# Optimization experiments

Hardware: AMD Instinct MI355X
Metric: run time of the kernel (lower is better)

The kernel has to match this reference:

```python
import jax, jax.numpy as jnp
import numpy as np

L = 2        # n_layers
D = 128      # embed_dim
H = 4        # n_heads
HD = D // H  # head_dim
B = 2
N = 4096
PERIOD = 2.0
WINDOW = 0.5
EPS = 1e-5
NF = D // 4  # n_frequencies = embed_dim / (n_dimensions * 2), n_dimensions=2


def setup_inputs() -> dict:
    key = jax.random.key(0)
    ks = jax.random.split(key, 12)
    s = 0.05  # weight init scale
    inp = {
        'x': jax.random.normal(ks[0], (B, N, D), jnp.float32),
        'pos': jax.random.uniform(ks[1], (B, N, 2), jnp.float32),
        'Wq_w': jax.random.normal(ks[2], (L, D, D), jnp.float32) * s,
        'Wq_b': jnp.zeros((L, D), jnp.float32),
        'Wk_w': jax.random.normal(ks[3], (L, D, D), jnp.float32) * s,
        'Wk_b': jnp.zeros((L, D), jnp.float32),
        'Wv_w': jax.random.normal(ks[4], (L, D, D), jnp.float32) * s,
        'Wv_b': jnp.zeros((L, D), jnp.float32),
        'Wo_w': jax.random.normal(ks[5], (L, D, D), jnp.float32) * s,
        'Wo_b': jnp.zeros((L, D), jnp.float32),
        'n1_g': jnp.ones((L, D), jnp.float32),
        'n1_b': jnp.zeros((L, D), jnp.float32),
        'n2_g': jnp.ones((L, D), jnp.float32),
        'n2_b': jnp.zeros((L, D), jnp.float32),
        'l1_w': jax.random.normal(ks[6], (L, D, 2 * D), jnp.float32) * s,
        'l1_b': jnp.zeros((L, 2 * D), jnp.float32),
        'l2_w': jax.random.normal(ks[7], (L, 2 * D, D), jnp.float32) * s,
        'l2_b': jnp.zeros((L, D), jnp.float32),
    }
    return inp


def _batchnorm(x, g, b):
    # BatchNorm1d in training mode over flattened (B*N, D)
    Bb, Nn, Dd = x.shape
    x2 = x.reshape(Bb * Nn, Dd)
    mu = x2.mean(0)
    var = x2.var(0)
    y = (x2 - mu) * jax.lax.rsqrt(var + EPS) * g + b
    return y.reshape(Bb, Nn, Dd)


def _rope(x, pos, freqs):
    # x: (B,N,D), pos: (B,N,2), freqs: (NF,)
    angle = pos[..., None] * freqs            # (B,N,2,NF)
    angle = jnp.repeat(angle, 2, axis=-1)     # (B,N,2,2*NF)
    angle = angle.reshape(x.shape)            # (B,N,D)
    xp = x.reshape(*x.shape[:-1], D // 2, 2)
    x_sw = jnp.stack([-xp[..., 1], xp[..., 0]], axis=-1).reshape(x.shape)
    return jnp.cos(angle) * x + jnp.sin(angle) * x_sw


def _forward(x, pos, Wq_w, Wq_b, Wk_w, Wk_b, Wv_w, Wv_b, Wo_w, Wo_b,
             n1_g, n1_b, n2_g, n2_b, l1_w, l1_b, l2_w, l2_b):
    freqs = 2 * jnp.pi * jnp.arange(1, NF + 1, dtype=x.dtype) / PERIOD
    # window mask: dist(i,j) <= WINDOW/2  -> compare squared distances
    sq = jnp.sum(pos * pos, axis=-1)                          # (B,N)
    d2 = sq[:, :, None] + sq[:, None, :] - 2 * jnp.einsum('bnd,bmd->bnm', pos, pos)
    mask = (d2 <= (WINDOW / 2) ** 2)[:, None, :, :]           # (B,1,N,N)
    scale = 1.0 / jnp.sqrt(jnp.asarray(HD, x.dtype))

    for i in range(L):
        xn = _batchnorm(x, n1_g[i], n1_b[i])
        q = xn @ Wq_w[i] + Wq_b[i]
        k = xn @ Wk_w[i] + Wk_b[i]
        v = xn @ Wv_w[i] + Wv_b[i]
        if i == 0:  # rotary encoding applied at first layer only
            q = _rope(q, pos, freqs)
            k = _rope(k, pos, freqs)
        # split heads: (B,N,D) -> (B,H,N,HD)
        qh = q.reshape(B, N, H, HD).transpose(0, 2, 1, 3)
        kh = k.reshape(B, N, H, HD).transpose(0, 2, 1, 3)
        vh = v.reshape(B, N, H, HD).transpose(0, 2, 1, 3)
        scores = jnp.einsum('bhnd,bhmd->bhnm', qh, kh) * scale
        scores = jnp.where(mask, scores, jnp.finfo(x.dtype).min)
        attn = jax.nn.softmax(scores, axis=-1)
        oh = jnp.einsum('bhnm,bhmd->bhnd', attn, vh)
        o = oh.transpose(0, 2, 1, 3).reshape(B, N, D)
        x = x + (o @ Wo_w[i] + Wo_b[i])
        # FFN block
        xn2 = _batchnorm(x, n2_g[i], n2_b[i])
        h = jax.nn.relu(xn2 @ l1_w[i] + l1_b[i])
        x = x + (h @ l2_w[i] + l2_b[i])
    return x


def reference(x, pos, Wq_w, Wq_b, Wk_w, Wk_b, Wv_w, Wv_b, Wo_w, Wo_b,
              n1_g, n1_b, n2_g, n2_b, l1_w, l1_b, l2_w, l2_b):
    return _forward(x, pos, Wq_w, Wq_b, Wk_w, Wk_b, Wv_w, Wv_b, Wo_w, Wo_b,
                    n1_g, n1_b, n2_g, n2_b, l1_w, l1_b, l2_w, l2_b)
```

## Files before the change

### kernel.cpp

```cpp
#include <hip/hip_runtime.h>
#include <hip/hip_bf16.h>
#include <math.h>

#define LYR 2
#define DIM 128
#define NH 4
#define HD 32
#define BB 2
#define NN 4096
#define MROWS (BB * NN)
#define R2 0.0625f
#define BN_EPS 1e-5f
#define CLOG2E 0.25503594f
#define NCH 4
#define CHLEN (NN / NCH)

typedef __attribute__((ext_vector_type(4))) float f32x4;
typedef __attribute__((ext_vector_type(8))) short bf16x8;
typedef __attribute__((ext_vector_type(4))) short bf16x4;

static __device__ inline unsigned short f2bf(float f) {
  union { float f; unsigned u; } v; v.f = f;
  unsigned r = v.u + 0x7FFFu + ((v.u >> 16) & 1u);
  return (unsigned short)(r >> 16);
}

static __device__ inline float exp2_fast(float x) {
#if defined(__has_builtin)
#if __has_builtin(__builtin_amdgcn_exp2f)
  return __builtin_amdgcn_exp2f(x);
#else
  return exp2f(x);
#endif
#else
  return exp2f(x);
#endif
}

static __device__ inline unsigned cvt_pk_bf16(float lo, float hi) {
  unsigned r;
  asm volatile("v_cvt_pk_bf16_f32 %0, %1, %2" : "=v"(r) : "v"(lo), "v"(hi));
  return r;
}

__global__ __launch_bounds__(256) void wprep_k(const float* __restrict__ Wq,
                                               const float* __restrict__ Wk,
                                               const float* __restrict__ Wv,
                                               const float* __restrict__ Wo,
                                               const float* __restrict__ L1,
                                               const float* __restrict__ L2,
                                               const float* __restrict__ Wqb,
                                               const float* __restrict__ Wkb,
                                               const float* __restrict__ Wvb,
                                               short* __restrict__ wT,
                                               float* __restrict__ qkvb) {
  const int id = blockIdx.x;
  const int l = id >> 7, r = id & 127;
  const size_t lbase = (size_t)l * 131072;
  const float* src; short* dst; int K, N, tk, tn;
  float mult = 1.0f;
  if (r < 64) {
    const int m = r >> 4, tile = r & 15;
    if (m == 0)      { src = Wq + (size_t)l * 16384; mult = CLOG2E; }
    else if (m == 1) src = Wk + (size_t)l * 16384;
    else if (m == 2) src = Wv + (size_t)l * 16384;
    else             src = Wo + (size_t)l * 16384;
    dst = wT + lbase + (size_t)m * 16384;
    K = 128; N = 128; tk = tile >> 2; tn = tile & 3;
  } else if (r < 96) {
    const int tile = r - 64;
    src = L1 + (size_t)l * 32768; dst = wT + lbase + 65536;
    K = 128; N = 256; tk = tile >> 3; tn = tile & 7;
  } else {
    const int tile = r - 96;
    src = L2 + (size_t)l * 32768; dst = wT + lbase + 98304;
    K = 256; N = 128; tk = tile >> 2; tn = tile & 3;
  }
  __shared__ float tl[32][33];
  const int t = threadIdx.x;
  const int rr = t >> 3, c4 = (t & 7) * 4;
  float4 vv = *(const float4*)(src + (size_t)(tk * 32 + rr) * N + tn * 32 + c4);
  tl[rr][c4 + 0] = vv.x; tl[rr][c4 + 1] = vv.y;
  tl[rr][c4 + 2] = vv.z; tl[rr][c4 + 3] = vv.w;
  __syncthreads();
  bf16x4 o4;
  o4[0] = (short)f2bf(tl[c4 + 0][rr] * mult);
  o4[1] = (short)f2bf(tl[c4 + 1][rr] * mult);
  o4[2] = (short)f2bf(tl[c4 + 2][rr] * mult);
  o4[3] = (short)f2bf(tl[c4 + 3][rr] * mult);
  *(bf16x4*)(dst + (size_t)(tn * 32 + rr) * K + tk * 32 + c4) = o4;
  if (r == 0) {
    for (int i = t; i < 384; i += 256) {
      float bv;
      if (i < 128)      bv = Wqb[l * 128 + i] * CLOG2E;
      else if (i < 256) bv = Wkb[l * 128 + i - 128];
      else              bv = Wvb[l * 128 + i - 256];
      qkvb[l * 384 + i] = bv;
    }
  }
}

__global__ __launch_bounds__(256) void copy_stats_k(const float* __restrict__ x,
                                                    float* __restrict__ out,
                                                    float* __restrict__ sums) {
  __shared__ float ss[8][128], sq[8][128];
  const int t = threadIdx.x;
  const int c4 = (t & 31) * 4, rg = t >> 5;
  const size_t base = (size_t)blockIdx.x * (32 * DIM);
  float s0 = 0.f, s1 = 0.f, s2 = 0.f, s3 = 0.f;
  float q0 = 0.f, q1 = 0.f, q2 = 0.f, q3 = 0.f;
  for (int r = rg; r < 32; r += 8) {
    float4 v = *(const float4*)&x[base + (size_t)r * DIM + c4];
    *(float4*)&out[base + (size_t)r * DIM + c4] = v;
    s0 += v.x; q0 += v.x * v.x;
    s1 += v.y; q1 += v.y * v.y;
    s2 += v.z; q2 += v.z * v.z;
    s3 += v.w; q3 += v.w * v.w;
  }
  ss[rg][c4 + 0] = s0; sq[rg][c4 + 0] = q0;
  ss[rg][c4 + 1] = s1; sq[rg][c4 + 1] = q1;
  ss[rg][c4 + 2] = s2; sq[rg][c4 + 2] = q2;
  ss[rg][c4 + 3] = s3; sq[rg][c4 + 3] = q3;
  __syncthreads();
  if (t < 128) {
    float S = 0.f, Q = 0.f;
#pragma unroll
    for (int r2 = 0; r2 < 8; r2++) { S += ss[r2][t]; Q += sq[r2][t]; }
    atomicAdd(&sums[t], S);
    atomicAdd(&sums[128 + t], Q);
  }
}

template <int MODE, bool RELU, bool ABN>
__global__ __launch_bounds__(256) void gemm_bf_k(const short* __restrict__ A,
                                                 const float* __restrict__ Af,
                                                 const float* __restrict__ stats,
                                                 const float* __restrict__ gma,
                                                 const float* __restrict__ btaN,
                                                 const short* __restrict__ WT,
                                                 const float* __restrict__ bias,
                                                 const float* res,
                                                 float* Cf,
                                                 short* __restrict__ Cb,
                                                 float* __restrict__ statsums,
                                                 int K) {
  __shared__ short a_s[64 * 80];
  __shared__ short w_s[64 * 80];
  __shared__ float sc_s[128], sh_s[128];
  const int t = threadIdx.x, w = t >> 6, lane = t & 63, g = lane >> 4, i16 = lane & 15;
  const int bm = blockIdx.x * 64, bn = blockIdx.y * 64;
  const int sr = t >> 2, sc = (t & 3) * 8, c16 = (t & 3) * 16;
  const size_t MN = (size_t)MROWS * DIM;
  if (ABN) {
    if (t < 128) {
      const float inv = 1.0f / (float)MROWS;
      const float mu = stats[t] * inv;
      const float var = stats[128 + t] * inv - mu * mu;
      const float rs = rsqrtf(var + BN_EPS);
      const float s = rs * gma[t];
      sc_s[t] = s;
      sh_s[t] = btaN[t] - mu * s;
    }
  }
  f32x4 acc[4];
#pragma unroll
  for (int ct = 0; ct < 4; ct++) acc[ct] = (f32x4){0.f, 0.f, 0.f, 0.f};
  for (int k0 = 0; k0 < K; k0 += 64) {
    __syncthreads();
    if (ABN) {
      const float* ap = Af + (size_t)(bm + sr) * K + k0 + c16;
      float4 x0 = *(const float4*)ap, x1 = *(const float4*)(ap + 4);
      float4 x2 = *(const float4*)(ap + 8), x3 = *(const float4*)(ap + 12);
      const int kb = k0 + c16;
      bf16x8 o0, o1;
      o0[0] = (short)f2bf(x0.x * sc_s[kb + 0]  + sh_s[kb + 0]);
      o0[1] = (short)f2bf(x0.y * sc_s[kb + 1]  + sh_s[kb + 1]);
      o0[2] = (short)f2bf(x0.z * sc_s[kb + 2]  + sh_s[kb + 2]);
      o0[3] = (short)f2bf(x0.w * sc_s[kb + 3]  + sh_s[kb + 3]);
      o0[4] = (short)f2bf(x1.x * sc_s[kb + 4]  + sh_s[kb + 4]);
      o0[5] = (short)f2bf(x1.y * sc_s[kb + 5]  + sh_s[kb + 5]);
      o0[6] = (short)f2bf(x1.z * sc_s[kb + 6]  + sh_s[kb + 6]);
      o0[7] = (short)f2bf(x1.w * sc_s[kb + 7]  + sh_s[kb + 7]);
      o1[0] = (short)f2bf(x2.x * sc_s[kb + 8]  + sh_s[kb + 8]);
      o1[1] = (short)f2bf(x2.y * sc_s[kb + 9]  + sh_s[kb + 9]);
      o1[2] = (short)f2bf(x2.z * sc_s[kb + 10] + sh_s[kb + 10]);
      o1[3] = (short)f2bf(x2.w * sc_s[kb + 11] + sh_s[kb + 11]);
      o1[4] = (short)f2bf(x3.x * sc_s[kb + 12] + sh_s[kb + 12]);
      o1[5] = (short)f2bf(x3.y * sc_s[kb + 13] + sh_s[kb + 13]);
      o1[6] = (short)f2bf(x3.z * sc_s[kb + 14] + sh_s[kb + 14]);
      o1[7] = (short)f2bf(x3.w * sc_s[kb + 15] + sh_s[kb + 15]);
      *(bf16x8*)&a_s[sr * 80 + c16] = o0;
      *(bf16x8*)&a_s[sr * 80 + c16 + 8] = o1;
    } else {
      *(bf16x8*)&a_s[sr * 80 + sc]      = *(const bf16x8*)(A + (size_t)(bm + sr) * K + k0 + sc);
      *(bf16x8*)&a_s[sr * 80 + sc + 32] = *(const bf16x8*)(A + (size_t)(bm + sr) * K + k0 + sc + 32);
    }
    *(bf16x8*)&w_s[sr * 80 + sc]      = *(const bf16x8*)(WT + (size_t)(bn + sr) * K + k0 + sc);
    *(bf16x8*)&w_s[sr * 80 + sc + 32] = *(const bf16x8*)(WT + (size_t)(bn + sr) * K + k0 + sc + 32);
    __syncthreads();
#pragma unroll
    for (int ks = 0; ks < 2; ks++) {
      bf16x8 af = *(const bf16x8*)&a_s[(16 * w + i16) * 80 + ks * 32 + 8 * g];
#pragma unroll
      for (int ct = 0; ct < 4; ct++) {
        bf16x8 wf = *(const bf16x8*)&w_s[(ct * 16 + i16) * 80 + ks * 32 + 8 * g];
        acc[ct] = __builtin_amdgcn_mfma_f32_16x16x32_bf16(af, wf, acc[ct], 0, 0, 0);
      }
    }
  }
  float s_acc[4], q_acc[4];
#pragma unroll
  for (int ct = 0; ct < 4; ct++) {
    const int col = bn + ct * 16 + i16;
    const float bv = bias[col];
    if (MODE == 3) {
      const int row0 = bm + 16 * w + 4 * g;
      if (col < 256) {
        short* dstb = (col < 128) ? Cb : (Cb + MN);
        const int cc = col & 127;
#pragma unroll
        for (int r = 0; r < 4; r++)
          dstb[(size_t)(row0 + r) * DIM + cc] = (short)f2bf(acc[ct][r] + bv);
      } else {
        const int b_ = row0 >> 12, n_ = row0 & (NN - 1);
        const int hh = (col - 256) >> 5, dd = (col - 256) & 31;
        bf16x4 o4;
#pragma unroll
        for (int r = 0; r < 4; r++) o4[r] = (short)f2bf(acc[ct][r] + bv);
        *(bf16x4*)(Cb + 2 * MN + ((size_t)(b_ * NH + hh) * HD + dd) * NN + n_) = o4;
      }
    } else if (MODE == 0) {
      float ssum = 0.f, qsum = 0.f;
#pragma unroll
      for (int r = 0; r < 4; r++) {
        const int row = bm + 16 * w + 4 * g + r;
        float vv = acc[ct][r] + bv + res[(size_t)row * DIM + col];
        Cf[(size_t)row * DIM + col] = vv;
        ssum += vv; qsum += vv * vv;
      }
      s_acc[ct] = ssum; q_acc[ct] = qsum;
    } else {
#pragma unroll
      for (int r = 0; r < 4; r++) {
        const int row = bm + 16 * w + 4 * g + r;
        float vv = acc[ct][r] + bv;
        if (RELU) vv = fmaxf(vv, 0.f);
        Cb[(size_t)row * (size_t)256 + col] = (short)f2bf(vv);
      }
    }
  }
  if (MODE == 0) {
#pragma unroll
    for (int ct = 0; ct < 4; ct++) {
      s_acc[ct] += __shfl_xor(s_acc[ct], 16, 64);
      s_acc[ct] += __shfl_xor(s_acc[ct], 32, 64);
      q_acc[ct] += __shfl_xor(q_acc[ct], 16, 64);
      q_acc[ct] += __shfl_xor(q_acc[ct], 32, 64);
    }
    float* bs = (float*)a_s;
    __syncthreads();
    if (t < 128) bs[t] = 0.f;
    __syncthreads();
    if (lane < 16) {
#pragma unroll
      for (int ct = 0; ct < 4; ct++) {
        atomicAdd(&bs[ct * 16 + i16], s_acc[ct]);
        atomicAdd(&bs[64 + ct * 16 + i16], q_acc[ct]);
      }
    }
    __syncthreads();
    if (t < 64) {
      atomicAdd(&statsums[bn + t], bs[t]);
      atomicAdd(&statsums[128 + bn + t], bs[64 + t]);
    }
  }
}

__global__ __launch_bounds__(256) void rope_bf_k(short* __restrict__ q,
                                                 short* __restrict__ kk,
                                                 const float* __restrict__ pos) {
  const int idx = blockIdx.x * 256 + threadIdx.x;
  const int row = idx >> 2, hh = idx & 3;
  const float2 pp = *(const float2*)&pos[(size_t)row * 2];
  short* qp = q + (size_t)row * DIM + hh * HD;
  short* kp = kk + (size_t)row * DIM + hh * HD;
  bf16x8 qv[4], kv[4];
#pragma unroll
  for (int u = 0; u < 4; u++) {
    qv[u] = *(const bf16x8*)(qp + 8 * u);
    kv[u] = *(const bf16x8*)(kp + 8 * u);
  }
#pragma unroll
  for (int lp = 0; lp < 16; lp++) {
    const int p = hh * 16 + lp;
    const float coord = (p < 32) ? pp.x : pp.y;
    const int f = p & 31;
    float sn, cs;
    __sincosf(3.14159265358979323846f * (float)(f + 1) * coord, &sn, &cs);
    const int u = lp >> 2, e = (lp & 3) * 2;
    const float a0 = __uint_as_float(((unsigned)(unsigned short)qv[u][e]) << 16);
    const float a1 = __uint_as_float(((unsigned)(unsigned short)qv[u][e + 1]) << 16);
    qv[u][e]     = (short)f2bf(cs * a0 - sn * a1);
    qv[u][e + 1] = (short)f2bf(cs * a1 + sn * a0);
    const float b0 = __uint_as_float(((unsigned)(unsigned short)kv[u][e]) << 16);
    const float b1 = __uint_as_float(((unsigned)(unsigned short)kv[u][e + 1]) << 16);
    kv[u][e]     = (short)f2bf(cs * b0 - sn * b1);
    kv[u][e + 1] = (short)f2bf(cs * b1 + sn * b0);
  }
#pragma unroll
  for (int u = 0; u < 4; u++) {
    *(bf16x8*)(qp + 8 * u) = qv[u];
    *(bf16x8*)(kp + 8 * u) = kv[u];
  }
}

__global__ __launch_bounds__(128) void attn4_k(const short* __restrict__ q,
                                               const short* __restrict__ k,
                                               const short* __restrict__ vt,
                                               const float* __restrict__ pos,
                                               float* __restrict__ accP,
                                               float* __restrict__ lP) {
  const int bh = blockIdx.y, b = bh >> 2, h = bh & 3;
  const int q0 = blockIdx.x * 32;
  const int ch = blockIdx.z;
  const int kbeg = ch * CHLEN, kend = kbeg + CHLEN;
  __shared__ short ks_s[64 * 40];
  __shared__ short vt_s[32 * 72];
  __shared__ short ps_s[2 * 16 * 72];
  __shared__ float pkx[64], pky[64], pnt[64];
  const int t = threadIdx.x, w = t >> 6, lane = t & 63, g = lane >> 4, i16 = lane & 15;
  const short* kp = k + (size_t)b * NN * DIM + h * HD;
  const short* vp = vt + (size_t)bh * HD * NN;

  const bf16x8 qf = *(const bf16x8*)(q + (size_t)(b * NN + q0 + 16 * w + i16) * DIM + h * HD + 8 * g);
  const float2 qp2 = *(const float2*)&pos[((size_t)b * NN + q0 + 16 * w + i16) * 2];
  const float qx = qp2.x, qy = qp2.y;
  const float ci = 0.5f * (qx * qx + qy * qy) - 0.5f * R2;

  bf16x8 kreg0 = *(const bf16x8*)(kp + (size_t)(kbeg + (t >> 2)) * DIM + (t & 3) * 8);
  bf16x8 kreg1 = *(const bf16x8*)(kp + (size_t)(kbeg + 32 + (t >> 2)) * DIM + (t & 3) * 8);
  bf16x8 vreg0 = *(const bf16x8*)(vp + (size_t)(t >> 3) * NN + kbeg + (t & 7) * 8);
  bf16x8 vreg1 = *(const bf16x8*)(vp + (size_t)((t >> 3) + 16) * NN + kbeg + (t & 7) * 8);
  float2 kpos = make_float2(0.f, 0.f);
  if (t < 64) kpos = *(const float2*)&pos[((size_t)b * NN + kbeg + t) * 2];

  f32x4 acc0 = {0.f, 0.f, 0.f, 0.f}, acc1 = {0.f, 0.f, 0.f, 0.f};
  const f32x4 zf = {0.f, 0.f, 0.f, 0.f};
  float l_run = 0.f;

  for (int k0 = kbeg; k0 < kend; k0 += 64) {
    __syncthreads();
    *(bf16x8*)&ks_s[(t >> 2) * 40 + (t & 3) * 8] = kreg0;
    *(bf16x8*)&ks_s[((t >> 2) + 32) * 40 + (t & 3) * 8] = kreg1;
    *(bf16x8*)&vt_s[(t >> 3) * 72 + (t & 7) * 8] = vreg0;
    *(bf16x8*)&vt_s[((t >> 3) + 16) * 72 + (t & 7) * 8] = vreg1;
    if (t < 64) {
      pkx[t] = kpos.x; pky[t] = kpos.y;
      pnt[t] = -0.5f * (kpos.x * kpos.x + kpos.y * kpos.y);
    }
    __syncthreads();
    const int kn = k0 + 64;
    if (kn < kend) {
      kreg0 = *(const bf16x8*)(kp + (size_t)(kn + (t >> 2)) * DIM + (t & 3) * 8);
      kreg1 = *(const bf16x8*)(kp + (size_t)(kn + 32 + (t >> 2)) * DIM + (t & 3) * 8);
      vreg0 = *(const bf16x8*)(vp + (size_t)(t >> 3) * NN + kn + (t & 7) * 8);
      vreg1 = *(const bf16x8*)(vp + (size_t)((t >> 3) + 16) * NN + kn + (t & 7) * 8);
      if (t < 64) kpos = *(const float2*)&pos[((size_t)b * NN + kn + t) * 2];
    }

    f32x4 sx[4];
#pragma unroll
    for (int jt = 0; jt < 4; jt++) {
      bf16x8 kf = *(const bf16x8*)&ks_s[(16 * jt + i16) * 40 + 8 * g];
      sx[jt] = __builtin_amdgcn_mfma_f32_16x16x32_bf16(kf, qf, zf, 0, 0, 0);
    }

    float pr[16];
    float tsum = 0.f;
#pragma unroll
    for (int jt = 0; jt < 4; jt++) {
      float4 kx4 = *(const float4*)&pkx[16 * jt + 4 * g];
      float4 ky4 = *(const float4*)&pky[16 * jt + 4 * g];
      float4 nt4 = *(const float4*)&pnt[16 * jt + 4 * g];
      const float kxa[4] = {kx4.x, kx4.y, kx4.z, kx4.w};
      const float kya[4] = {ky4.x, ky4.y, ky4.z, ky4.w};
      const float nta[4] = {nt4.x, nt4.y, nt4.z, nt4.w};
#pragma unroll
      for (int r = 0; r < 4; r++) {
        const float dot = fmaf(qx, kxa[r], fmaf(qy, kya[r], nta[r]));
        float p = exp2_fast(sx[jt][r]);
        p = (dot >= ci) ? p : 0.f;
        pr[jt * 4 + r] = p;
        tsum += p;
      }
    }
    l_run += tsum;

#pragma unroll
    for (int jt = 0; jt < 4; jt++) {
      uint2 w2;
      w2.x = cvt_pk_bf16(pr[jt * 4 + 0], pr[jt * 4 + 1]);
      w2.y = cvt_pk_bf16(pr[jt * 4 + 2], pr[jt * 4 + 3]);
      *(uint2*)&ps_s[w * 1152 + i16 * 72 + 16 * jt + 4 * g] = w2;
    }

#pragma unroll
    for (int ks2 = 0; ks2 < 2; ks2++) {
      bf16x8 pf = *(const bf16x8*)&ps_s[w * 1152 + i16 * 72 + 8 * g + 32 * ks2];
      bf16x8 vf0 = *(const bf16x8*)&vt_s[i16 * 72 + 8 * g + 32 * ks2];
      bf16x8 vf1 = *(const bf16x8*)&vt_s[(16 + i16) * 72 + 8 * g + 32 * ks2];
      acc0 = __builtin_amdgcn_mfma_f32_16x16x32_bf16(pf, vf0, acc0, 0, 0, 0);
      acc1 = __builtin_amdgcn_mfma_f32_16x16x32_bf16(pf, vf1, acc1, 0, 0, 0);
    }
  }

  l_run += __shfl_xor(l_run, 16, 64);
  l_run += __shfl_xor(l_run, 32, 64);
  if (lane < 16)
    lP[(size_t)(ch * 8 + bh) * NN + q0 + 16 * w + lane] = l_run;
  float* ap = accP + ((size_t)(ch * 8 + bh) * NN + q0 + 16 * w) * HD;
#pragma unroll
  for (int r = 0; r < 4; r++) {
    ap[(4 * g + r) * HD + i16] = acc0[r];
    ap[(4 * g + r) * HD + 16 + i16] = acc1[r];
  }
}

__global__ __launch_bounds__(256) void attn_comb_k(const float* __restrict__ accP,
                                                   const float* __restrict__ lP,
                                                   short* __restrict__ ob) {
  const int idx = blockIdx.x * 256 + threadIdx.x;
  const int b = idx >> 17;
  const int n = (idx >> 5) & (NN - 1);
  const int hd = idx & 31;
  const int h = hd >> 3, d4 = (hd & 7) * 4;
  const int bh = b * NH + h;
  float ax = 0.f, ay = 0.f, az = 0.f, aw = 0.f, l = 0.f;
#pragma unroll
  for (int c = 0; c < NCH; c++) {
    const float4 v = *(const float4*)&accP[((size_t)(c * 8 + bh) * NN + n) * HD + d4];
    ax += v.x; ay += v.y; az += v.z; aw += v.w;
    l += lP[(size_t)(c * 8 + bh) * NN + n];
  }
  const float inv = 1.0f / l;
  bf16x4 o;
  o[0] = (short)f2bf(ax * inv);
  o[1] = (short)f2bf(ay * inv);
  o[2] = (short)f2bf(az * inv);
  o[3] = (short)f2bf(aw * inv);
  *(bf16x4*)&ob[((size_t)b * NN + n) * DIM + h * HD + d4] = o;
}

extern "C" void kernel_launch(void* const* d_in, const int* in_sizes, int n_in,
                              void* d_out, int out_size, void* d_ws, size_t ws_size,
                              hipStream_t stream) {
  const float* x = (const float*)d_in[0];
  const float* pos = (const float*)d_in[1];
  const float* Wq_w = (const float*)d_in[2];
  const float* Wq_b = (const float*)d_in[3];
  const float* Wk_w = (const float*)d_in[4];
  const float* Wk_b = (const float*)d_in[5];
  const float* Wv_w = (const float*)d_in[6];
  const float* Wv_b = (const float*)d_in[7];
  const float* Wo_w = (const float*)d_in[8];
  const float* Wo_b = (const float*)d_in[9];
  const float* n1_g = (const float*)d_in[10];
  const float* n1_b = (const float*)d_in[11];
  const float* n2_g = (const float*)d_in[12];
  const float* n2_b = (const float*)d_in[13];
  const float* l1_w = (const float*)d_in[14];
  const float* l1_b = (const float*)d_in[15];
  const float* l2_w = (const float*)d_in[16];
  const float* l2_b = (const float*)d_in[17];

  float* out = (float*)d_out;
  short* wsS = (short*)d_ws;
  const size_t MN = (size_t)MROWS * DIM;
  short* qb_bf = wsS;
  short* ob_bf = wsS + 3 * MN;
  short* wT    = wsS + 4 * MN;
  float* fbase = (float*)(wsS + 4 * MN + 262144);
  float* qkvb  = fbase;
  float* sums  = fbase + 768;
  float* lP    = fbase + 2048;
  float* accP  = fbase + 2048 + 131072;
  short* hb_bf = (short*)accP;

  wprep_k<<<256, 256, 0, stream>>>(Wq_w, Wk_w, Wv_w, Wo_w, l1_w, l2_w,
                                   Wq_b, Wk_b, Wv_b, wT, qkvb);
  hipMemsetAsync(sums, 0, 1280 * sizeof(float), stream);
  copy_stats_k<<<256, 256, 0, stream>>>(x, out, sums);

  for (int l = 0; l < LYR; l++) {
    const short* lw = wT + (size_t)l * 131072;
    float* s_n1 = sums + (2 * l) * 256;
    float* s_n2 = sums + (2 * l + 1) * 256;
    float* s_nx = sums + (2 * l + 2) * 256;

    gemm_bf_k<3, false, true><<<dim3(128, 6), 256, 0, stream>>>(
        nullptr, out, s_n1, n1_g + l * DIM, n1_b + l * DIM,
        lw, qkvb + l * 384, nullptr, nullptr, qb_bf, nullptr, 128);
    if (l == 0) rope_bf_k<<<128, 256, 0, stream>>>(qb_bf, qb_bf + MN, pos);
    attn4_k<<<dim3(NN / 32, BB * NH, NCH), 128, 0, stream>>>(
        qb_bf, qb_bf + MN, qb_bf + 2 * MN, pos, accP, lP);
    attn_comb_k<<<1024, 256, 0, stream>>>(accP, lP, ob_bf);
    gemm_bf_k<0, false, false><<<dim3(128, 2), 256, 0, stream>>>(
        ob_bf, nullptr, nullptr, nullptr, nullptr,
        lw + 49152, Wo_b + l * DIM, out, out, nullptr, s_n2, 128);

    gemm_bf_k<1, true, true><<<dim3(128, 4), 256, 0, stream>>>(
        nullptr, out, s_n2, n2_g + l * DIM, n2_b + l * DIM,
        lw + 65536, l1_b + l * 2 * DIM, nullptr, nullptr, hb_bf, nullptr, 128);
    gemm_bf_k<0, false, false><<<dim3(128, 2), 256, 0, stream>>>(
        hb_bf, nullptr, nullptr, nullptr, nullptr,
        lw + 98304, l2_b + l * DIM, out, out, nullptr, s_nx, 256);
  }
}
```

Baseline: 308.1 us.

## Rewrite attention kernel to load K/V straight into registers, two query tiles per wave

Replaces the LDS-staged attention kernel with one that reads K and V fragments directly from global memory into MFMA operands. Each wave now handles two 16-query tiles so every K/V fragment feeds two MFMAs, and the probabilities stay in registers as the B operand instead of going through shared memory. Key positions and their squared norms are precomputed once into a float4 array in the copy/stats kernel. This removes LDS traffic and barriers but relies on the cache to absorb repeated global K/V reads across blocks.

```diff
diff --git a/kernel.cpp b/kernel.cpp
--- a/kernel.cpp
+++ b/kernel.cpp
@@ -102,7 +102,9 @@
 
 __global__ __launch_bounds__(256) void copy_stats_k(const float* __restrict__ x,
                                                     float* __restrict__ out,
-                                                    float* __restrict__ sums) {
+                                                    float* __restrict__ sums,
+                                                    const float* __restrict__ pos,
+                                                    float* __restrict__ pposG) {
   __shared__ float ss[8][128], sq[8][128];
   const int t = threadIdx.x;
   const int c4 = (t & 31) * 4, rg = t >> 5;
@@ -116,6 +118,12 @@
     s1 += v.y; q1 += v.y * v.y;
     s2 += v.z; q2 += v.z * v.z;
     s3 += v.w; q3 += v.w * v.w;
+  }
+  if (t < 32) {
+    const int row = blockIdx.x * 32 + t;
+    float2 pp2 = *(const float2*)&pos[(size_t)row * 2];
+    float4 o4 = make_float4(pp2.x, pp2.y, -0.5f * (pp2.x * pp2.x + pp2.y * pp2.y), 0.f);
+    *(float4*)&pposG[(size_t)row * 4] = o4;
   }
   ss[rg][c4 + 0] = s0; sq[rg][c4 + 0] = q0;
   ss[rg][c4 + 1] = s1; sq[rg][c4 + 1] = q1;
@@ -314,115 +322,101 @@
   }
 }
 
-__global__ __launch_bounds__(128) void attn4_k(const short* __restrict__ q,
+__global__ __launch_bounds__(256) void attn5_k(const short* __restrict__ q,
                                                const short* __restrict__ k,
                                                const short* __restrict__ vt,
-                                               const float* __restrict__ pos,
+                                               const float* __restrict__ pposG,
                                                float* __restrict__ accP,
                                                float* __restrict__ lP) {
   const int bh = blockIdx.y, b = bh >> 2, h = bh & 3;
-  const int q0 = blockIdx.x * 32;
   const int ch = blockIdx.z;
-  const int kbeg = ch * CHLEN, kend = kbeg + CHLEN;
-  __shared__ short ks_s[64 * 40];
-  __shared__ short vt_s[32 * 72];
-  __shared__ short ps_s[2 * 16 * 72];
-  __shared__ float pkx[64], pky[64], pnt[64];
+  const int kbeg = ch * CHLEN;
   const int t = threadIdx.x, w = t >> 6, lane = t & 63, g = lane >> 4, i16 = lane & 15;
+  const int q0w = blockIdx.x * 128 + w * 32;
   const short* kp = k + (size_t)b * NN * DIM + h * HD;
   const short* vp = vt + (size_t)bh * HD * NN;
-
-  const bf16x8 qf = *(const bf16x8*)(q + (size_t)(b * NN + q0 + 16 * w + i16) * DIM + h * HD + 8 * g);
-  const float2 qp2 = *(const float2*)&pos[((size_t)b * NN + q0 + 16 * w + i16) * 2];
-  const float qx = qp2.x, qy = qp2.y;
-  const float ci = 0.5f * (qx * qx + qy * qy) - 0.5f * R2;
-
-  bf16x8 kreg0 = *(const bf16x8*)(kp + (size_t)(kbeg + (t >> 2)) * DIM + (t & 3) * 8);
-  bf16x8 kreg1 = *(const bf16x8*)(kp + (size_t)(kbeg + 32 + (t >> 2)) * DIM + (t & 3) * 8);
-  bf16x8 vreg0 = *(const bf16x8*)(vp + (size_t)(t >> 3) * NN + kbeg + (t & 7) * 8);
-  bf16x8 vreg1 = *(const bf16x8*)(vp + (size_t)((t >> 3) + 16) * NN + kbeg + (t & 7) * 8);
-  float2 kpos = make_float2(0.f, 0.f);
-  if (t < 64) kpos = *(const float2*)&pos[((size_t)b * NN + kbeg + t) * 2];
-
-  f32x4 acc0 = {0.f, 0.f, 0.f, 0.f}, acc1 = {0.f, 0.f, 0.f, 0.f};
+  const float4* pp = (const float4*)pposG + (size_t)b * NN;
+
+  bf16x8 qf[2];
+  float qx[2], qy[2], ci[2];
+#pragma unroll
+  for (int a = 0; a < 2; a++) {
+    const int nq = q0w + 16 * a + i16;
+    qf[a] = *(const bf16x8*)(q + (size_t)(b * NN + nq) * DIM + h * HD + 8 * g);
+    const float4 qp4 = pp[nq];
+    qx[a] = qp4.x; qy[a] = qp4.y;
+    ci[a] = -qp4.z - 0.5f * R2;
+  }
+  const int jbase = 8 * (i16 >> 2) + (i16 & 3);
+  f32x4 acc[2][2];
+#pragma unroll
+  for (int a = 0; a < 2; a++)
+#pragma unroll
+    for (int dh = 0; dh < 2; dh++) acc[a][dh] = (f32x4){0.f, 0.f, 0.f, 0.f};
+  float lr[2] = {0.f, 0.f};
   const f32x4 zf = {0.f, 0.f, 0.f, 0.f};
-  float l_run = 0.f;
-
-  for (int k0 = kbeg; k0 < kend; k0 += 64) {
-    __syncthreads();
-    *(bf16x8*)&ks_s[(t >> 2) * 40 + (t & 3) * 8] = kreg0;
-    *(bf16x8*)&ks_s[((t >> 2) + 32) * 40 + (t & 3) * 8] = kreg1;
-    *(bf16x8*)&vt_s[(t >> 3) * 72 + (t & 7) * 8] = vreg0;
-    *(bf16x8*)&vt_s[((t >> 3) + 16) * 72 + (t & 7) * 8] = vreg1;
-    if (t < 64) {
-      pkx[t] = kpos.x; pky[t] = kpos.y;
-      pnt[t] = -0.5f * (kpos.x * kpos.x + kpos.y * kpos.y);
-    }
-    __syncthreads();
-    const int kn = k0 + 64;
-    if (kn < kend) {
-      kreg0 = *(const bf16x8*)(kp + (size_t)(kn + (t >> 2)) * DIM + (t & 3) * 8);
-      kreg1 = *(const bf16x8*)(kp + (size_t)(kn + 32 + (t >> 2)) * DIM + (t & 3) * 8);
-      vreg0 = *(const bf16x8*)(vp + (size_t)(t >> 3) * NN + kn + (t & 7) * 8);
-      vreg1 = *(const bf16x8*)(vp + (size_t)((t >> 3) + 16) * NN + kn + (t & 7) * 8);
-      if (t < 64) kpos = *(const float2*)&pos[((size_t)b * NN + kn + t) * 2];
-    }
-
-    f32x4 sx[4];
+
+  for (int k0 = kbeg; k0 < kbeg + CHLEN; k0 += 64) {
+    bf16x8 kf[4];
+    kf[0] = *(const bf16x8*)(kp + (size_t)(k0 + jbase + 0) * DIM + 8 * g);
+    kf[1] = *(const bf16x8*)(kp + (size_t)(k0 + jbase + 4) * DIM + 8 * g);
+    kf[2] = *(const bf16x8*)(kp + (size_t)(k0 + jbase + 32) * DIM + 8 * g);
+    kf[3] = *(const bf16x8*)(kp + (size_t)(k0 + jbase + 36) * DIM + 8 * g);
+
+    f32x4 sx[2][4];
 #pragma unroll
     for (int jt = 0; jt < 4; jt++) {
-      bf16x8 kf = *(const bf16x8*)&ks_s[(16 * jt + i16) * 40 + 8 * g];
-      sx[jt] = __builtin_amdgcn_mfma_f32_16x16x32_bf16(kf, qf, zf, 0, 0, 0);
-    }
-
-    float pr[16];
-    float tsum = 0.f;
+      sx[0][jt] = __builtin_amdgcn_mfma_f32_16x16x32_bf16(kf[jt], qf[0], zf, 0, 0, 0);
+      sx[1][jt] = __builtin_amdgcn_mfma_f32_16x16x32_bf16(kf[jt], qf[1], zf, 0, 0, 0);
+    }
+
+    unsigned pk[2][8];
 #pragma unroll
     for (int jt = 0; jt < 4; jt++) {
-      float4 kx4 = *(const float4*)&pkx[16 * jt + 4 * g];
-      float4 ky4 = *(const float4*)&pky[16 * jt + 4 * g];
-      float4 nt4 = *(const float4*)&pnt[16 * jt + 4 * g];
-      const float kxa[4] = {kx4.x, kx4.y, kx4.z, kx4.w};
-      const float kya[4] = {ky4.x, ky4.y, ky4.z, ky4.w};
-      const float nta[4] = {nt4.x, nt4.y, nt4.z, nt4.w};
-#pragma unroll
-      for (int r = 0; r < 4; r++) {
-        const float dot = fmaf(qx, kxa[r], fmaf(qy, kya[r], nta[r]));
-        float p = exp2_fast(sx[jt][r]);
-        p = (dot >= ci) ? p : 0.f;
-        pr[jt * 4 + r] = p;
-        tsum += p;
-      }
-    }
-    l_run += tsum;
-
-#pragma unroll
-    for (int jt = 0; jt < 4; jt++) {
-      uint2 w2;
-      w2.x = cvt_pk_bf16(pr[jt * 4 + 0], pr[jt * 4 + 1]);
-      w2.y = cvt_pk_bf16(pr[jt * 4 + 2], pr[jt * 4 + 3]);
-      *(uint2*)&ps_s[w * 1152 + i16 * 72 + 16 * jt + 4 * g] = w2;
-    }
-
-#pragma unroll
-    for (int ks2 = 0; ks2 < 2; ks2++) {
-      bf16x8 pf = *(const bf16x8*)&ps_s[w * 1152 + i16 * 72 + 8 * g + 32 * ks2];
-      bf16x8 vf0 = *(const bf16x8*)&vt_s[i16 * 72 + 8 * g + 32 * ks2];
-      bf16x8 vf1 = *(const bf16x8*)&vt_s[(16 + i16) * 72 + 8 * g + 32 * ks2];
-      acc0 = __builtin_amdgcn_mfma_f32_16x16x32_bf16(pf, vf0, acc0, 0, 0, 0);
-      acc1 = __builtin_amdgcn_mfma_f32_16x16x32_bf16(pf, vf1, acc1, 0, 0, 0);
-    }
-  }
-
-  l_run += __shfl_xor(l_run, 16, 64);
-  l_run += __shfl_xor(l_run, 32, 64);
-  if (lane < 16)
-    lP[(size_t)(ch * 8 + bh) * NN + q0 + 16 * w + lane] = l_run;
-  float* ap = accP + ((size_t)(ch * 8 + bh) * NN + q0 + 16 * w) * HD;
-#pragma unroll
-  for (int r = 0; r < 4; r++) {
-    ap[(4 * g + r) * HD + i16] = acc0[r];
-    ap[(4 * g + r) * HD + 16 + i16] = acc1[r];
+      const int jo = k0 + ((jt >> 1) << 5) + ((jt & 1) << 2) + 8 * g;
+      float4 pj0 = pp[jo + 0], pj1 = pp[jo + 1], pj2 = pp[jo + 2], pj3 = pp[jo + 3];
+#pragma unroll
+      for (int a = 0; a < 2; a++) {
+        float p0 = exp2_fast(sx[a][jt][0]);
+        float p1 = exp2_fast(sx[a][jt][1]);
+        float p2 = exp2_fast(sx[a][jt][2]);
+        float p3 = exp2_fast(sx[a][jt][3]);
+        p0 = (fmaf(qx[a], pj0.x, fmaf(qy[a], pj0.y, pj0.z)) >= ci[a]) ? p0 : 0.f;
+        p1 = (fmaf(qx[a], pj1.x, fmaf(qy[a], pj1.y, pj1.z)) >= ci[a]) ? p1 : 0.f;
+        p2 = (fmaf(qx[a], pj2.x, fmaf(qy[a], pj2.y, pj2.z)) >= ci[a]) ? p2 : 0.f;
+        p3 = (fmaf(qx[a], pj3.x, fmaf(qy[a], pj3.y, pj3.z)) >= ci[a]) ? p3 : 0.f;
+        lr[a] += (p0 + p1) + (p2 + p3);
+        pk[a][jt * 2 + 0] = cvt_pk_bf16(p0, p1);
+        pk[a][jt * 2 + 1] = cvt_pk_bf16(p2, p3);
+      }
+    }
+
+#pragma unroll
+    for (int jh = 0; jh < 2; jh++) {
+      union { unsigned u[4]; bf16x8 v; } pf0, pf1;
+#pragma unroll
+      for (int u = 0; u < 4; u++) { pf0.u[u] = pk[0][jh * 4 + u]; pf1.u[u] = pk[1][jh * 4 + u]; }
+#pragma unroll
+      for (int dh = 0; dh < 2; dh++) {
+        bf16x8 vf = *(const bf16x8*)(vp + (size_t)(dh * 16 + i16) * NN + k0 + jh * 32 + 8 * g);
+        acc[0][dh] = __builtin_amdgcn_mfma_f32_16x16x32_bf16(vf, pf0.v, acc[0][dh], 0, 0, 0);
+        acc[1][dh] = __builtin_amdgcn_mfma_f32_16x16x32_bf16(vf, pf1.v, acc[1][dh], 0, 0, 0);
+      }
+    }
+  }
+
+#pragma unroll
+  for (int a = 0; a < 2; a++) {
+    lr[a] += __shfl_xor(lr[a], 16, 64);
+    lr[a] += __shfl_xor(lr[a], 32, 64);
+    if (lane < 16)
+      lP[(size_t)(ch * 8 + bh) * NN + q0w + 16 * a + lane] = lr[a];
+    float* ap = accP + ((size_t)(ch * 8 + bh) * NN + q0w + 16 * a + i16) * HD;
+#pragma unroll
+    for (int dh = 0; dh < 2; dh++)
+#pragma unroll
+      for (int r = 0; r < 4; r++)
+        ap[dh * 16 + 4 * g + r] = acc[a][dh][r];
   }
 }
 
@@ -484,12 +478,13 @@
   float* sums  = fbase + 768;
   float* lP    = fbase + 2048;
   float* accP  = fbase + 2048 + 131072;
+  float* pposG = accP + 4194304;
   short* hb_bf = (short*)accP;
 
   wprep_k<<<256, 256, 0, stream>>>(Wq_w, Wk_w, Wv_w, Wo_w, l1_w, l2_w,
                                    Wq_b, Wk_b, Wv_b, wT, qkvb);
   hipMemsetAsync(sums, 0, 1280 * sizeof(float), stream);
-  copy_stats_k<<<256, 256, 0, stream>>>(x, out, sums);
+  copy_stats_k<<<256, 256, 0, stream>>>(x, out, sums, pos, pposG);
 
   for (int l = 0; l < LYR; l++) {
     const short* lw = wT + (size_t)l * 131072;
@@ -501,8 +496,8 @@
         nullptr, out, s_n1, n1_g + l * DIM, n1_b + l * DIM,
         lw, qkvb + l * 384, nullptr, nullptr, qb_bf, nullptr, 128);
     if (l == 0) rope_bf_k<<<128, 256, 0, stream>>>(qb_bf, qb_bf + MN, pos);
-    attn4_k<<<dim3(NN / 32, BB * NH, NCH), 128, 0, stream>>>(
-        qb_bf, qb_bf + MN, qb_bf + 2 * MN, pos, accP, lP);
+    attn5_k<<<dim3(NN / 128, BB * NH, NCH), 256, 0, stream>>>(
+        qb_bf, qb_bf + MN, qb_bf + 2 * MN, pposG, accP, lP);
     attn_comb_k<<<1024, 256, 0, stream>>>(accP, lP, ob_bf);
     gemm_bf_k<0, false, false><<<dim3(128, 2), 256, 0, stream>>>(
         ob_bf, nullptr, nullptr, nullptr, nullptr,
```

After: 398.8 us. 1.29x slower.
